# Kernel tuning notes

Hardware: AMD Instinct MI355X
Metric: run time of the kernel (lower is better)

## Reference

```python
import jax, jax.numpy as jnp
import numpy as np

K = 3  # number of nearest neighbors for interpolation
BIG = 1e10  # masks out cross-batch pairs in the distance matrix


def setup_inputs() -> dict:
    key = jax.random.key(0)
    ks = jax.random.split(key, 8)
    N, Ns, C, Cs, B = 4096, 16384, 256, 128, 4
    Din, H = C + Cs, 256
    return {
        "x": jax.random.normal(ks[0], (N, C), dtype=jnp.float32),
        "pos": jax.random.normal(ks[1], (N, 3), dtype=jnp.float32),
        "batch": jnp.sort(jax.random.randint(ks[2], (N,), 0, B)),
        "x_skip": jax.random.normal(ks[3], (Ns, Cs), dtype=jnp.float32),
        "pos_skip": jax.random.normal(ks[4], (Ns, 3), dtype=jnp.float32),
        "batch_skip": jnp.sort(jax.random.randint(ks[5], (Ns,), 0, B)),
        "W1": jax.random.normal(ks[6], (Din, H), dtype=jnp.float32) * (1.0 / np.sqrt(Din)),
        "b1": jnp.zeros((H,), dtype=jnp.float32),
        "W2": jax.random.normal(ks[7], (H, H), dtype=jnp.float32) * (1.0 / np.sqrt(H)),
        "b2": jnp.zeros((H,), dtype=jnp.float32),
    }


def reference(x, pos, batch, x_skip, pos_skip, batch_skip, W1, b1, W2, b2):
    # knn_interpolate: squared distances from each fine point to all coarse points,
    # masked so neighbors only come from the same batch element.
    d2 = jnp.sum((pos_skip[:, None, :] - pos[None, :, :]) ** 2, axis=-1)  # [Ns, N]
    d2 = jnp.where(batch_skip[:, None] != batch[None, :], BIG, d2)
    neg_d2, idx = jax.lax.top_k(-d2, K)          # k smallest distances, [Ns, K]
    w = 1.0 / jnp.clip(-neg_d2, 1e-16)           # inverse-squared-distance weights
    num = jnp.sum(x[idx] * w[..., None], axis=1)  # [Ns, C] weighted gather-reduce
    y = num / jnp.sum(w, axis=1, keepdims=True)
    # concat skip features, then MLP (Linear-ReLU-Linear-ReLU)
    y = jnp.concatenate([y, x_skip], axis=1)      # [Ns, C + Cs]
    h = jax.nn.relu(y @ W1 + b1)
    out = jax.nn.relu(h @ W2 + b2)
    return (out, pos_skip, batch_skip)
```

## Files before the change

### kernel.cpp

```cpp
#include <hip/hip_runtime.h>
#include <stdint.h>

#define NPTS   4096
#define NSKIP  16384
#define CCH    256
#define CSK    128
#define DIN    384
#define HDIM   256
#define BIGF   1e10f

typedef unsigned short u16;
typedef __attribute__((ext_vector_type(8))) short short8;
typedef __attribute__((ext_vector_type(4))) float floatx4;

__device__ __forceinline__ u16 f2bf(float f) {
    union { float f; uint32_t u; } c; c.f = f;
    uint32_t u = c.u;
    return (u16)((u + 0x7FFFu + ((u >> 16) & 1u)) >> 16);
}

__device__ __forceinline__ double pkkey(float d, int j) {
    return __hiloint2double(__float_as_int(d), j);
}

__global__ __launch_bounds__(256) void prep_kernel(
    const float* __restrict__ W1, const float* __restrict__ W2,
    u16* __restrict__ W1p, u16* __restrict__ W2p,
    const float* __restrict__ pos, float4* __restrict__ pos4)
{
    const int bid = blockIdx.x;
    const int t = threadIdx.x;

    const float* W = (bid < 48) ? W1 : W2;
    u16* Wp       = (bid < 48) ? W1p : W2p;
    const int KT  = (bid < 48) ? 12 : 8;
    const int g   = ((bid < 48) ? bid : (bid - 48)) * 256 + t;

    const int lane = g & 63;
    const int kt = (g >> 6) % KT;
    const int nt = (g >> 6) / KT;
    const int kbase = kt * 32 + (lane >> 4) * 8;
    const int n = nt * 16 + (lane & 15);
    u16 v[8];
#pragma unroll
    for (int j = 0; j < 8; ++j) v[j] = f2bf(W[(size_t)(kbase + j) * HDIM + n]);
#pragma unroll
    for (int j = 0; j < 8; ++j) Wp[(size_t)g * 8 + j] = v[j];

    if (bid >= 48 && bid < 64) {
        const int p = (bid - 48) * 256 + t;
        pos4[p] = make_float4(pos[p * 3 + 0], pos[p * 3 + 1], pos[p * 3 + 2], 0.0f);
    }
}

__global__ __launch_bounds__(1024, 8) void mega_kernel(
    const float* __restrict__ x, const float* __restrict__ x_skip,
    const float4* __restrict__ pos4, const int* __restrict__ batch,
    const u16* __restrict__ W1p, const float* __restrict__ b1,
    const u16* __restrict__ W2p, const float* __restrict__ b2,
    const float* __restrict__ pos_skip, const int* __restrict__ batch_skip,
    float* __restrict__ out)
{
    __shared__ u16 sA[32 * 392];
    __shared__ float sOut[32 * 256];
    __shared__ int   sIdx[32 * 3];
    __shared__ float sWgt[32 * 3];
    __shared__ int   sRange[5];
    const int t = threadIdx.x;
    const int row0 = blockIdx.x * 32;
    const int wave = t >> 6, lane = t & 63;
    const int quad = lane >> 4, ml = lane & 15;

    if (t < 5) {
        int lo = 0, hi = NPTS;
        while (lo < hi) {
            const int m = (lo + hi) >> 1;
            if (batch[m] < t) lo = m + 1; else hi = m;
        }
        sRange[t] = lo;
    }
    {
        const int row = t >> 5, c4 = t & 31;
        const float4 v = *(const float4*)(x_skip + (size_t)(row0 + row) * CSK + c4 * 4);
        uint2 pk;
        pk.x = (uint32_t)f2bf(v.x) | ((uint32_t)f2bf(v.y) << 16);
        pk.y = (uint32_t)f2bf(v.z) | ((uint32_t)f2bf(v.w) << 16);
        *(uint2*)(sA + row * 392 + CCH + c4 * 4) = pk;
    }
    __syncthreads();

    {
        const int rl = t >> 5;
        const int sub = t & 31;
        const int i = row0 + rl;
        const int b = batch_skip[i];
        const int start = sRange[b], end = sRange[b + 1];

        const float px = pos_skip[i * 3 + 0];
        const float py = pos_skip[i * 3 + 1];
        const float pz = pos_skip[i * 3 + 2];

        const double BIGKEY = pkkey(BIGF, 0x7FFFFFFF);
        double k0 = BIGKEY, k1 = BIGKEY, k2 = BIGKEY;

        for (int j = start + sub; j < end; j += 32) {
            const float4 q = pos4[j];
            const float dx = __fsub_rn(px, q.x);
            const float dy = __fsub_rn(py, q.y);
            const float dz = __fsub_rn(pz, q.z);
            const float dd = __fadd_rn(__fadd_rn(__fmul_rn(dx, dx), __fmul_rn(dy, dy)),
                                       __fmul_rn(dz, dz));
            const double kk = pkkey(dd, j);
            const double u0 = fmax(k0, kk); k0 = fmin(k0, kk);
            const double u1 = fmax(k1, u0); k1 = fmin(k1, u0);
            k2 = fmin(k2, u1);
        }

#pragma unroll
        for (int m = 1; m < 32; m <<= 1) {
            const double o0 = __shfl_xor(k0, m);
            const double o1 = __shfl_xor(k1, m);
            const double o2 = __shfl_xor(k2, m);
            double u0 = fmax(k0, o0); k0 = fmin(k0, o0);
            double u1 = fmax(k1, u0); k1 = fmin(k1, u0);
            k2 = fmin(k2, u1);
            u1 = fmax(k1, o1); k1 = fmin(k1, o1);
            k2 = fmin(k2, u1);
            k2 = fmin(k2, o2);
        }

        if (sub == 0) {
            const float d0 = __int_as_float(__double2hiint(k0));
            const float d1 = __int_as_float(__double2hiint(k1));
            const float d2 = __int_as_float(__double2hiint(k2));
            const float w0 = 1.0f / fmaxf(d0, 1e-16f);
            const float w1 = 1.0f / fmaxf(d1, 1e-16f);
            const float w2 = 1.0f / fmaxf(d2, 1e-16f);
            const float inv = 1.0f / (w0 + w1 + w2);
            sIdx[rl * 3 + 0] = __double2loint(k0);
            sIdx[rl * 3 + 1] = __double2loint(k1);
            sIdx[rl * 3 + 2] = __double2loint(k2);
            sWgt[rl * 3 + 0] = w0 * inv;
            sWgt[rl * 3 + 1] = w1 * inv;
            sWgt[rl * 3 + 2] = w2 * inv;
        }
    }
    __syncthreads();

#pragma unroll
    for (int k = 0; k < 2; ++k) {
        const int g = t + 1024 * k;
        const int row = g >> 6, c4 = g & 63;
        const int i0 = sIdx[row * 3 + 0], i1 = sIdx[row * 3 + 1], i2 = sIdx[row * 3 + 2];
        const float w0 = sWgt[row * 3 + 0], w1 = sWgt[row * 3 + 1], w2 = sWgt[row * 3 + 2];
        const float4 v0 = *(const float4*)(x + (size_t)i0 * CCH + c4 * 4);
        const float4 v1 = *(const float4*)(x + (size_t)i1 * CCH + c4 * 4);
        const float4 v2 = *(const float4*)(x + (size_t)i2 * CCH + c4 * 4);
        const float a  = w0 * v0.x + w1 * v1.x + w2 * v2.x;
        const float bq = w0 * v0.y + w1 * v1.y + w2 * v2.y;
        const float cq = w0 * v0.z + w1 * v1.z + w2 * v2.z;
        const float dq = w0 * v0.w + w1 * v1.w + w2 * v2.w;
        uint2 pk;
        pk.x = (uint32_t)f2bf(a)  | ((uint32_t)f2bf(bq) << 16);
        pk.y = (uint32_t)f2bf(cq) | ((uint32_t)f2bf(dq) << 16);
        *(uint2*)(sA + row * 392 + c4 * 4) = pk;
    }
    __syncthreads();

    floatx4 acc[2] = {};
    {
        const u16* aA = sA + ml * 392 + quad * 8;
        for (int kt = 0; kt < 12; ++kt) {
            short8 a0 = *(const short8*)(aA + kt * 32);
            short8 a1 = *(const short8*)(aA + 16 * 392 + kt * 32);
            short8 bfr = *(const short8*)(W1p + (size_t)((wave * 12 + kt) * 64 + lane) * 8);
            acc[0] = __builtin_amdgcn_mfma_f32_16x16x32_bf16(a0, bfr, acc[0], 0, 0, 0);
            acc[1] = __builtin_amdgcn_mfma_f32_16x16x32_bf16(a1, bfr, acc[1], 0, 0, 0);
        }
    }
    __syncthreads();

    {
        const int n = wave * 16 + ml;
        const float bv = b1[n];
#pragma unroll
        for (int mt = 0; mt < 2; ++mt) {
#pragma unroll
            for (int r = 0; r < 4; ++r) {
                const int m = mt * 16 + quad * 4 + r;
                sA[m * 264 + n] = f2bf(fmaxf(acc[mt][r] + bv, 0.0f));
            }
        }
    }
    __syncthreads();

    floatx4 acc2[2] = {};
    {
        const u16* aH = sA + ml * 264 + quad * 8;
        for (int kt = 0; kt < 8; ++kt) {
            short8 a0 = *(const short8*)(aH + kt * 32);
            short8 a1 = *(const short8*)(aH + 16 * 264 + kt * 32);
            short8 bfr = *(const short8*)(W2p + (size_t)((wave * 8 + kt) * 64 + lane) * 8);
            acc2[0] = __builtin_amdgcn_mfma_f32_16x16x32_bf16(a0, bfr, acc2[0], 0, 0, 0);
            acc2[1] = __builtin_amdgcn_mfma_f32_16x16x32_bf16(a1, bfr, acc2[1], 0, 0, 0);
        }
    }

    {
        const int n = wave * 16 + ml;
        const float bv = b2[n];
#pragma unroll
        for (int mt = 0; mt < 2; ++mt) {
#pragma unroll
            for (int r = 0; r < 4; ++r) {
                const int m = mt * 16 + quad * 4 + r;
                sOut[m * 256 + n] = fmaxf(acc2[mt][r] + bv, 0.0f);
            }
        }
    }
    __syncthreads();
    {
        float* dst = out + (size_t)row0 * HDIM;
#pragma unroll
        for (int k = 0; k < 2; ++k) {
            const int e = t + 1024 * k;
            *(float4*)(dst + e * 4) = *(const float4*)(sOut + e * 4);
        }
    }

    if (t < 128) {
        const int e = blockIdx.x * 128 + t;
        const size_t base = (size_t)NSKIP * HDIM;
        if (e < NSKIP * 3) out[base + e] = pos_skip[e];
        else               out[base + e] = (float)batch_skip[e - NSKIP * 3];
    }
}

extern "C" void kernel_launch(void* const* d_in, const int* in_sizes, int n_in,
                              void* d_out, int out_size, void* d_ws, size_t ws_size,
                              hipStream_t stream) {
    const float* x         = (const float*)d_in[0];
    const float* pos       = (const float*)d_in[1];
    const int*   batch     = (const int*)d_in[2];
    const float* x_skip    = (const float*)d_in[3];
    const float* pos_skip  = (const float*)d_in[4];
    const int*   batch_skip= (const int*)d_in[5];
    const float* W1        = (const float*)d_in[6];
    const float* b1        = (const float*)d_in[7];
    const float* W2        = (const float*)d_in[8];
    const float* b2        = (const float*)d_in[9];
    float* out = (float*)d_out;

    char* ws = (char*)d_ws;
    u16*    W1p   = (u16*)ws;
    u16*    W2p   = (u16*)(ws + 196608);
    float4* pos4  = (float4*)(ws + 327680);

    prep_kernel<<<80, 256, 0, stream>>>(W1, W2, W1p, W2p, pos, pos4);
    mega_kernel<<<NSKIP / 32, 1024, 0, stream>>>(x, x_skip, pos4, batch,
                                                 W1p, b1, W2p, b2,
                                                 pos_skip, batch_skip, out);
}
```

Baseline: 108.7 us.

## Precompute batch ranges in prep kernel and fuse kNN with gather without barriers

Measured after the change: 109.0 us. No clear change (+0.2%).

```diff
diff --git a/kernel.cpp b/kernel.cpp
--- a/kernel.cpp
+++ b/kernel.cpp
@@ -26,7 +26,8 @@
 __global__ __launch_bounds__(256) void prep_kernel(
     const float* __restrict__ W1, const float* __restrict__ W2,
     u16* __restrict__ W1p, u16* __restrict__ W2p,
-    const float* __restrict__ pos, float4* __restrict__ pos4)
+    const float* __restrict__ pos, float4* __restrict__ pos4,
+    const int* __restrict__ batch, int* __restrict__ range)
 {
     const int bid = blockIdx.x;
     const int t = threadIdx.x;
@@ -51,11 +52,27 @@
         const int p = (bid - 48) * 256 + t;
         pos4[p] = make_float4(pos[p * 3 + 0], pos[p * 3 + 1], pos[p * 3 + 2], 0.0f);
     }
+
+    if (bid == 0) {
+        for (int j = t * 16; j < t * 16 + 16; ++j) {
+            if (j == 0) {
+                const int b0 = batch[0];
+                for (int b = 0; b <= b0; ++b) range[b] = 0;
+            } else {
+                const int bp = batch[j - 1], bj = batch[j];
+                for (int b = bp + 1; b <= bj; ++b) range[b] = j;
+            }
+            if (j == NPTS - 1) {
+                const int bl = batch[NPTS - 1];
+                for (int b = bl + 1; b <= 4; ++b) range[b] = NPTS;
+            }
+        }
+    }
 }
 
 __global__ __launch_bounds__(1024, 8) void mega_kernel(
     const float* __restrict__ x, const float* __restrict__ x_skip,
-    const float4* __restrict__ pos4, const int* __restrict__ batch,
+    const float4* __restrict__ pos4, const int* __restrict__ range,
     const u16* __restrict__ W1p, const float* __restrict__ b1,
     const u16* __restrict__ W2p, const float* __restrict__ b2,
     const float* __restrict__ pos_skip, const int* __restrict__ batch_skip,
@@ -63,107 +80,91 @@
 {
     __shared__ u16 sA[32 * 392];
     __shared__ float sOut[32 * 256];
-    __shared__ int   sIdx[32 * 3];
-    __shared__ float sWgt[32 * 3];
-    __shared__ int   sRange[5];
     const int t = threadIdx.x;
     const int row0 = blockIdx.x * 32;
     const int wave = t >> 6, lane = t & 63;
     const int quad = lane >> 4, ml = lane & 15;
-
-    if (t < 5) {
-        int lo = 0, hi = NPTS;
-        while (lo < hi) {
-            const int m = (lo + hi) >> 1;
-            if (batch[m] < t) lo = m + 1; else hi = m;
-        }
-        sRange[t] = lo;
-    }
-    {
-        const int row = t >> 5, c4 = t & 31;
-        const float4 v = *(const float4*)(x_skip + (size_t)(row0 + row) * CSK + c4 * 4);
+    const int rl = t >> 5;
+    const int sub = t & 31;
+    const int i = row0 + rl;
+
+    const float4 vs = *(const float4*)(x_skip + (size_t)i * CSK + sub * 4);
+    const int b = batch_skip[i];
+    const int start = range[b], end = range[b + 1];
+    const float px = pos_skip[i * 3 + 0];
+    const float py = pos_skip[i * 3 + 1];
+    const float pz = pos_skip[i * 3 + 2];
+    {
         uint2 pk;
-        pk.x = (uint32_t)f2bf(v.x) | ((uint32_t)f2bf(v.y) << 16);
-        pk.y = (uint32_t)f2bf(v.z) | ((uint32_t)f2bf(v.w) << 16);
-        *(uint2*)(sA + row * 392 + CCH + c4 * 4) = pk;
-    }
-    __syncthreads();
-
-    {
-        const int rl = t >> 5;
-        const int sub = t & 31;
-        const int i = row0 + rl;
-        const int b = batch_skip[i];
-        const int start = sRange[b], end = sRange[b + 1];
-
-        const float px = pos_skip[i * 3 + 0];
-        const float py = pos_skip[i * 3 + 1];
-        const float pz = pos_skip[i * 3 + 2];
-
-        const double BIGKEY = pkkey(BIGF, 0x7FFFFFFF);
-        double k0 = BIGKEY, k1 = BIGKEY, k2 = BIGKEY;
-
-        for (int j = start + sub; j < end; j += 32) {
-            const float4 q = pos4[j];
-            const float dx = __fsub_rn(px, q.x);
-            const float dy = __fsub_rn(py, q.y);
-            const float dz = __fsub_rn(pz, q.z);
-            const float dd = __fadd_rn(__fadd_rn(__fmul_rn(dx, dx), __fmul_rn(dy, dy)),
-                                       __fmul_rn(dz, dz));
-            const double kk = pkkey(dd, j);
-            const double u0 = fmax(k0, kk); k0 = fmin(k0, kk);
-            const double u1 = fmax(k1, u0); k1 = fmin(k1, u0);
-            k2 = fmin(k2, u1);
-        }
-
-#pragma unroll
-        for (int m = 1; m < 32; m <<= 1) {
-            const double o0 = __shfl_xor(k0, m);
-            const double o1 = __shfl_xor(k1, m);
-            const double o2 = __shfl_xor(k2, m);
-            double u0 = fmax(k0, o0); k0 = fmin(k0, o0);
-            double u1 = fmax(k1, u0); k1 = fmin(k1, u0);
-            k2 = fmin(k2, u1);
-            u1 = fmax(k1, o1); k1 = fmin(k1, o1);
-            k2 = fmin(k2, u1);
-            k2 = fmin(k2, o2);
-        }
-
-        if (sub == 0) {
-            const float d0 = __int_as_float(__double2hiint(k0));
-            const float d1 = __int_as_float(__double2hiint(k1));
-            const float d2 = __int_as_float(__double2hiint(k2));
-            const float w0 = 1.0f / fmaxf(d0, 1e-16f);
-            const float w1 = 1.0f / fmaxf(d1, 1e-16f);
-            const float w2 = 1.0f / fmaxf(d2, 1e-16f);
-            const float inv = 1.0f / (w0 + w1 + w2);
-            sIdx[rl * 3 + 0] = __double2loint(k0);
-            sIdx[rl * 3 + 1] = __double2loint(k1);
-            sIdx[rl * 3 + 2] = __double2loint(k2);
-            sWgt[rl * 3 + 0] = w0 * inv;
-            sWgt[rl * 3 + 1] = w1 * inv;
-            sWgt[rl * 3 + 2] = w2 * inv;
-        }
-    }
-    __syncthreads();
-
-#pragma unroll
-    for (int k = 0; k < 2; ++k) {
-        const int g = t + 1024 * k;
-        const int row = g >> 6, c4 = g & 63;
-        const int i0 = sIdx[row * 3 + 0], i1 = sIdx[row * 3 + 1], i2 = sIdx[row * 3 + 2];
-        const float w0 = sWgt[row * 3 + 0], w1 = sWgt[row * 3 + 1], w2 = sWgt[row * 3 + 2];
-        const float4 v0 = *(const float4*)(x + (size_t)i0 * CCH + c4 * 4);
-        const float4 v1 = *(const float4*)(x + (size_t)i1 * CCH + c4 * 4);
-        const float4 v2 = *(const float4*)(x + (size_t)i2 * CCH + c4 * 4);
-        const float a  = w0 * v0.x + w1 * v1.x + w2 * v2.x;
-        const float bq = w0 * v0.y + w1 * v1.y + w2 * v2.y;
-        const float cq = w0 * v0.z + w1 * v1.z + w2 * v2.z;
-        const float dq = w0 * v0.w + w1 * v1.w + w2 * v2.w;
-        uint2 pk;
-        pk.x = (uint32_t)f2bf(a)  | ((uint32_t)f2bf(bq) << 16);
-        pk.y = (uint32_t)f2bf(cq) | ((uint32_t)f2bf(dq) << 16);
-        *(uint2*)(sA + row * 392 + c4 * 4) = pk;
+        pk.x = (uint32_t)f2bf(vs.x) | ((uint32_t)f2bf(vs.y) << 16);
+        pk.y = (uint32_t)f2bf(vs.z) | ((uint32_t)f2bf(vs.w) << 16);
+        *(uint2*)(sA + rl * 392 + CCH + sub * 4) = pk;
+    }
+
+    const double BIGKEY = pkkey(BIGF, 0x7FFFFFFF);
+    double k0 = BIGKEY, k1 = BIGKEY, k2 = BIGKEY;
+    for (int j = start + sub; j < end; j += 32) {
+        const float4 q = pos4[j];
+        const float dx = __fsub_rn(px, q.x);
+        const float dy = __fsub_rn(py, q.y);
+        const float dz = __fsub_rn(pz, q.z);
+        const float dd = __fadd_rn(__fadd_rn(__fmul_rn(dx, dx), __fmul_rn(dy, dy)),
+                                   __fmul_rn(dz, dz));
+        const double kk = pkkey(dd, j);
+        const double u0 = fmax(k0, kk); k0 = fmin(k0, kk);
+        const double u1 = fmax(k1, u0); k1 = fmin(k1, u0);
+        k2 = fmin(k2, u1);
+    }
+#pragma unroll
+    for (int m = 1; m < 32; m <<= 1) {
+        const double o0 = __shfl_xor(k0, m);
+        const double o1 = __shfl_xor(k1, m);
+        const double o2 = __shfl_xor(k2, m);
+        double u0 = fmax(k0, o0); k0 = fmin(k0, o0);
+        double u1 = fmax(k1, u0); k1 = fmin(k1, u0);
+        k2 = fmin(k2, u1);
+        u1 = fmax(k1, o1); k1 = fmin(k1, o1);
+        k2 = fmin(k2, u1);
+        k2 = fmin(k2, o2);
+    }
+
+    const int i0 = __double2loint(k0);
+    const int i1 = __double2loint(k1);
+    const int i2 = __double2loint(k2);
+    {
+        const float d0 = __int_as_float(__double2hiint(k0));
+        const float d1 = __int_as_float(__double2hiint(k1));
+        const float d2 = __int_as_float(__double2hiint(k2));
+        const float w0r = 1.0f / fmaxf(d0, 1e-16f);
+        const float w1r = 1.0f / fmaxf(d1, 1e-16f);
+        const float w2r = 1.0f / fmaxf(d2, 1e-16f);
+        const float inv = 1.0f / (w0r + w1r + w2r);
+        const float w0 = w0r * inv, w1 = w1r * inv, w2 = w2r * inv;
+
+        const float* xr0 = x + (size_t)i0 * CCH + sub * 8;
+        const float* xr1 = x + (size_t)i1 * CCH + sub * 8;
+        const float* xr2 = x + (size_t)i2 * CCH + sub * 8;
+        const float4 a0 = *(const float4*)(xr0);
+        const float4 a1 = *(const float4*)(xr0 + 4);
+        const float4 c0 = *(const float4*)(xr1);
+        const float4 c1 = *(const float4*)(xr1 + 4);
+        const float4 e0 = *(const float4*)(xr2);
+        const float4 e1 = *(const float4*)(xr2 + 4);
+
+        const float y0 = w0 * a0.x + w1 * c0.x + w2 * e0.x;
+        const float y1 = w0 * a0.y + w1 * c0.y + w2 * e0.y;
+        const float y2 = w0 * a0.z + w1 * c0.z + w2 * e0.z;
+        const float y3 = w0 * a0.w + w1 * c0.w + w2 * e0.w;
+        const float y4 = w0 * a1.x + w1 * c1.x + w2 * e1.x;
+        const float y5 = w0 * a1.y + w1 * c1.y + w2 * e1.y;
+        const float y6 = w0 * a1.z + w1 * c1.z + w2 * e1.z;
+        const float y7 = w0 * a1.w + w1 * c1.w + w2 * e1.w;
+        uint4 pk;
+        pk.x = (uint32_t)f2bf(y0) | ((uint32_t)f2bf(y1) << 16);
+        pk.y = (uint32_t)f2bf(y2) | ((uint32_t)f2bf(y3) << 16);
+        pk.z = (uint32_t)f2bf(y4) | ((uint32_t)f2bf(y5) << 16);
+        pk.w = (uint32_t)f2bf(y6) | ((uint32_t)f2bf(y7) << 16);
+        *(uint4*)(sA + rl * 392 + sub * 8) = pk;
     }
     __syncthreads();
 
@@ -254,10 +255,11 @@
     char* ws = (char*)d_ws;
     u16*    W1p   = (u16*)ws;
     u16*    W2p   = (u16*)(ws + 196608);
-    float4* pos4  = (float4*)(ws + 327680);
-
-    prep_kernel<<<80, 256, 0, stream>>>(W1, W2, W1p, W2p, pos, pos4);
-    mega_kernel<<<NSKIP / 32, 1024, 0, stream>>>(x, x_skip, pos4, batch,
+    int*    range = (int*)(ws + 327680);
+    float4* pos4  = (float4*)(ws + 327712);
+
+    prep_kernel<<<80, 256, 0, stream>>>(W1, W2, W1p, W2p, pos, pos4, batch, range);
+    mega_kernel<<<NSKIP / 32, 1024, 0, stream>>>(x, x_skip, pos4, range,
                                                  W1p, b1, W2p, b2,
                                                  pos_skip, batch_skip, out);
 }
```
